# Kernel optimization log

Hardware: AMD Instinct MI355X
Metric: run time of the kernel (lower is better)

## Reference

```python
import jax, jax.numpy as jnp
import numpy as np

N, P, CF, K = 64, 1024, 16, 16  # batch, points, feature channels (after stripping 2 coord dims), knn K
BN_EPS = 1e-5


def _bn(x, g, b, m, v):
    # channel-last batchnorm in eval mode
    return (x - m) / jnp.sqrt(v + BN_EPS) * g + b


def _knn(pts, k):
    # pts: (N,P,2) -> indices of k nearest neighbors excluding self: (N,P,k)
    r = jnp.sum(pts * pts, axis=-1)                      # (N,P)
    d = r[:, :, None] - 2.0 * jnp.einsum('npc,nqc->npq', pts, pts) + r[:, None, :]
    _, idx = jax.lax.top_k(-d, k + 1)                    # (N,P,k+1)
    return idx[:, :, 1:]


def setup_inputs() -> dict:
    key = jax.random.key(0)
    ks = jax.random.split(key, 8)
    inp = {
        'features': jax.random.normal(ks[0], (N, P, 2 + CF), dtype=jnp.float32),
        'mask': jnp.zeros((N, P), dtype=bool),
        # edge conv stack: Conv2d(32->64), Conv2d(64->64), Conv2d(64->64), all 1x1
        'W0': jax.random.normal(ks[1], (64, 2 * CF), dtype=jnp.float32) / np.sqrt(2 * CF),
        'W1': jax.random.normal(ks[2], (64, 64), dtype=jnp.float32) / 8.0,
        'W2': jax.random.normal(ks[3], (64, 64), dtype=jnp.float32) / 8.0,
        # shortcut Conv1d(16->64)
        'Ws': jax.random.normal(ks[4], (64, CF), dtype=jnp.float32) / np.sqrt(CF),
    }
    for i, kk in zip(['0', '1', '2', 's'], jax.random.split(ks[5], 4)):
        k1, k2 = jax.random.split(kk)
        inp['g' + i] = jnp.ones((64,), jnp.float32)
        inp['b' + i] = jnp.zeros((64,), jnp.float32)
        inp['m' + i] = 0.1 * jax.random.normal(k1, (64,), jnp.float32)
        inp['v' + i] = jnp.ones((64,), jnp.float32) + 0.1 * jax.random.uniform(k2, (64,))
    return inp


def reference(features, mask, W0, W1, W2, Ws,
              g0, b0, m0, v0, g1, b1, m1, v1, g2, b2, m2, v2, gs, bs, ms, vs):
    pts = features[..., :2]          # (N,P,2)
    X = features[..., 2:]            # (N,P,CF)
    X_shortcut = X

    idx = _knn(pts, K)               # (N,P,K)
    f = jax.vmap(lambda x, i: x[i])(X, idx)              # gather neighbors: (N,P,K,CF)
    fc = jnp.broadcast_to(X[:, :, None, :], f.shape)     # center tiled
    h = jnp.concatenate([fc, fc - f], axis=-1)           # (N,P,K,2*CF)

    valid = mask.shape[1] - jnp.sum(mask, axis=1)        # (N,) number of valid points
    mask_K = idx >= valid[:, None, None]                 # (N,P,K) neighbor is padding

    for W, g, b, m, v in ((W0, g0, b0, m0, v0), (W1, g1, b1, m1, v1), (W2, g2, b2, m2, v2)):
        h = jax.nn.relu(_bn(jnp.einsum('npkc,oc->npko', h, W), g, b, m, v))

    h = jnp.where(mask_K[..., None], 0.0, h)             # (N,P,K,64)
    denom = jnp.maximum((K - jnp.sum(mask_K, axis=2)).astype(h.dtype), 1e-8)[..., None]
    agg = jnp.sum(h, axis=2) / denom                     # masked mean over K: (N,P,64)

    sc = _bn(jnp.einsum('npc,oc->npo', X_shortcut, Ws), gs, bs, ms, vs)
    sc = jnp.where(mask[..., None], 0.0, sc)

    out = jax.nn.relu(agg + sc)                          # (N,P,64)
    return jnp.transpose(out, (0, 2, 1))                 # (N,64,P) to match torch layout
```

## Files before the change

kernel.cpp:

```cpp
#include <hip/hip_runtime.h>

#define N_P 1024
#define N_K 16
#define C_IN 18

typedef _Float16 f16;
typedef f16 f16x8 __attribute__((ext_vector_type(8)));
typedef f16 f16x4 __attribute__((ext_vector_type(4)));
typedef float f32x4 __attribute__((ext_vector_type(4)));
typedef unsigned long long u64;

__global__ __launch_bounds__(256, 3) void fused_kernel(
    const float* __restrict__ feat, const unsigned char* __restrict__ mask,
    const float* __restrict__ W0, const float* __restrict__ W1,
    const float* __restrict__ W2, const float* __restrict__ Ws,
    const float* __restrict__ g0, const float* __restrict__ b0,
    const float* __restrict__ m0, const float* __restrict__ v0,
    const float* __restrict__ g1, const float* __restrict__ b1,
    const float* __restrict__ m1, const float* __restrict__ v1,
    const float* __restrict__ g2, const float* __restrict__ b2,
    const float* __restrict__ m2, const float* __restrict__ v2,
    const float* __restrict__ gs, const float* __restrict__ bs,
    const float* __restrict__ ms, const float* __restrict__ vs,
    float* __restrict__ out) {

    __shared__ __align__(16) char sbytes[16640 + 34816 + 16];
    float4* spts = (float4*)sbytes;
    float (*fbuf)[65] = (float(*)[65])sbytes;
    double* part = (double*)(sbytes + 16640);
    f16 (*hb)[16][72] = (f16(*)[16][72])(sbytes + 16640);
    int (*idx_lds)[16] = (int(*)[16])(sbytes + 16640 + 9216);
    int* msum = (int*)(sbytes + 16640 + 34816);

    const int tid = threadIdx.x;
    const int lane = tid & 63;
    const int w = tid >> 6;
    const int g = lane >> 4;
    const int c15 = lane & 15;
    const int n = blockIdx.x >> 4;
    const int P0 = (blockIdx.x & 15) << 6;
    const int PB = P0 + (w << 4);

    const float* fB = feat + (size_t)n * N_P * C_IN;

    if (tid == 0) *msum = 0;
    __syncthreads();
    for (int i = tid; i < N_P; i += 256) {
        float x = fB[i * C_IN + 0];
        float y = fB[i * C_IN + 1];
        float r = __fadd_rn(__fmul_rn(x, x), __fmul_rn(y, y));
        spts[i] = make_float4(x, y, r, 0.f);
    }
    {
        unsigned int m4 = *(const unsigned int*)(mask + (size_t)n * N_P + tid * 4);
        int part_c = (int)(((m4 & 0xFFu) != 0) + (((m4 >> 8) & 0xFFu) != 0) +
                           (((m4 >> 16) & 0xFFu) != 0) + (((m4 >> 24) & 0xFFu) != 0));
        atomicAdd(msum, part_c);
    }
    __syncthreads();
    const int valid = N_P - *msum;

    {
        const int q = lane;
        const int base = w << 8;
        const float4 me = spts[P0 + q];
        const float px = me.x, py = me.y, rp = me.z;

        double kk[17];
#pragma unroll
        for (int j = 0; j < 17; ++j) kk[j] = 0x1.0p60;

        double idx_d = (double)base;
        float4 nq = spts[base];
        for (int i = 0; i < 256; ++i) {
            const float4 qc = nq;
            nq = spts[base + ((i + 1) & 255)];
            float dot = __fadd_rn(__fmul_rn(px, qc.x), __fmul_rn(py, qc.y));
            float d   = __fadd_rn(__fsub_rn(rp, __fmul_rn(2.f, dot)), qc.z);
            unsigned int ud = __float_as_uint(d);
            ud ^= (unsigned int)((int)ud >> 31) | 0x80000000u;
            double x = fma((double)ud, 1024.0, idx_d);
            idx_d += 1.0;
#pragma unroll
            for (int j = 0; j < 17; ++j) {
                double lo = fmin(kk[j], x);
                x = fmax(kk[j], x);
                kk[j] = lo;
            }
        }
        double* pp = part + ((w << 6) + q) * 17;
#pragma unroll
        for (int j = 0; j < 17; ++j) pp[j] = kk[j];
    }
    __syncthreads();

    double fk[17];
    const bool owner = (lane < 16);
    {
#pragma unroll
        for (int j = 0; j < 17; ++j) fk[j] = 0x1.0p60;
        if (owner) {
            const int q = (w << 4) + lane;
            for (int s = 0; s < 4; ++s) {
                const double* pp = part + ((s << 6) + q) * 17;
#pragma unroll
                for (int j = 0; j < 17; ++j) {
                    double x = pp[j];
#pragma unroll
                    for (int jj = 0; jj < 17; ++jj) {
                        double lo = fmin(fk[jj], x);
                        x = fmax(fk[jj], x);
                        fk[jj] = lo;
                    }
                }
            }
        }
    }
    __syncthreads();
    if (owner) {
        const int q = (w << 4) + lane;
#pragma unroll
        for (int j = 1; j < 17; ++j) {
            double hi = trunc(fk[j] * 0x1.0p-10);
            idx_lds[q][j - 1] = (int)(fk[j] - hi * 1024.0);
        }
    }

    float tb0[4], tb1[4], tb2[4], tbs[4];
    f16x8 w0f[4], w1f[4][2], w2f[4][2];
    f16x4 wsf[4];
#pragma unroll
    for (int t = 0; t < 4; ++t) {
        const int o = t * 16 + c15;
        float s0 = g0[o] / sqrtf(v0[o] + 1e-5f);  tb0[t] = b0[o] - m0[o] * s0;
        float s1 = g1[o] / sqrtf(v1[o] + 1e-5f);  tb1[t] = b1[o] - m1[o] * s1;
        float s2 = g2[o] / sqrtf(v2[o] + 1e-5f);  tb2[t] = b2[o] - m2[o] * s2;
        float ss = gs[o] / sqrtf(vs[o] + 1e-5f);  tbs[t] = bs[o] - ms[o] * ss;
        const float* w0r = W0 + o * 32 + g * 8;
#pragma unroll
        for (int e = 0; e < 8; ++e) w0f[t][e] = (f16)(w0r[e] * s0);
        const float* w1r = W1 + o * 64 + g * 8;
        const float* w2r = W2 + o * 64 + g * 8;
#pragma unroll
        for (int ch = 0; ch < 2; ++ch)
#pragma unroll
            for (int e = 0; e < 8; ++e) {
                w1f[t][ch][e] = (f16)(w1r[ch * 32 + e] * s1);
                w2f[t][ch][e] = (f16)(w2r[ch * 32 + e] * s2);
            }
        const float* wsr = Ws + o * 16 + g * 4;
#pragma unroll
        for (int e = 0; e < 4; ++e) wsf[t][e] = (f16)(wsr[e] * ss);
    }

    for (int pp = 0; pp < 16; ++pp) {
        const int p = PB + pp;
        const int* ip = idx_lds[(w << 4) + pp];

        const int q = ip[c15];
        const int half = g & 1;
        const float* fcp = fB + p * C_IN + 2 + half * 8;
        float e0[8];
#pragma unroll
        for (int j = 0; j < 4; ++j) {
            float2 v = *(const float2*)(fcp + 2 * j);
            e0[2 * j] = v.x; e0[2 * j + 1] = v.y;
        }
        if (g >= 2) {
            const float* fqp = fB + q * C_IN + 2 + half * 8;
#pragma unroll
            for (int j = 0; j < 4; ++j) {
                float2 v = *(const float2*)(fqp + 2 * j);
                e0[2 * j] -= v.x; e0[2 * j + 1] -= v.y;
            }
        }
        f16x8 a0;
#pragma unroll
        for (int j = 0; j < 8; ++j) a0[j] = (f16)e0[j];

        f32x4 acc[4];
#pragma unroll
        for (int t = 0; t < 4; ++t) {
            acc[t] = (f32x4){tb0[t], tb0[t], tb0[t], tb0[t]};
            acc[t] = __builtin_amdgcn_mfma_f32_16x16x32_f16(a0, w0f[t], acc[t], 0, 0, 0);
        }
#pragma unroll
        for (int t = 0; t < 4; ++t)
#pragma unroll
            for (int r = 0; r < 4; ++r)
                hb[w][4 * g + r][t * 16 + c15] = (f16)fmaxf(acc[t][r], 0.f);

        f16x8 a1a = *(const f16x8*)&hb[w][c15][g * 8];
        f16x8 a1b = *(const f16x8*)&hb[w][c15][32 + g * 8];
        f32x4 acc1[4];
#pragma unroll
        for (int t = 0; t < 4; ++t) {
            acc1[t] = (f32x4){tb1[t], tb1[t], tb1[t], tb1[t]};
            acc1[t] = __builtin_amdgcn_mfma_f32_16x16x32_f16(a1a, w1f[t][0], acc1[t], 0, 0, 0);
            acc1[t] = __builtin_amdgcn_mfma_f32_16x16x32_f16(a1b, w1f[t][1], acc1[t], 0, 0, 0);
        }
#pragma unroll
        for (int t = 0; t < 4; ++t)
#pragma unroll
            for (int r = 0; r < 4; ++r)
                hb[w][4 * g + r][t * 16 + c15] = (f16)fmaxf(acc1[t][r], 0.f);

        f16x8 a2a = *(const f16x8*)&hb[w][c15][g * 8];
        f16x8 a2b = *(const f16x8*)&hb[w][c15][32 + g * 8];
        f32x4 acc2[4];
#pragma unroll
        for (int t = 0; t < 4; ++t) {
            acc2[t] = (f32x4){tb2[t], tb2[t], tb2[t], tb2[t]};
            acc2[t] = __builtin_amdgcn_mfma_f32_16x16x32_f16(a2a, w2f[t][0], acc2[t], 0, 0, 0);
            acc2[t] = __builtin_amdgcn_mfma_f32_16x16x32_f16(a2b, w2f[t][1], acc2[t], 0, 0, 0);
        }
        float ssum[4] = {0.f, 0.f, 0.f, 0.f};
        int cnt = 0;
#pragma unroll
        for (int r = 0; r < 4; ++r) {
            int qq = ip[4 * g + r];
            bool fl = (qq >= valid);
            cnt += fl ? 1 : 0;
#pragma unroll
            for (int t = 0; t < 4; ++t) {
                float v = fmaxf(acc2[t][r], 0.f);
                ssum[t] += fl ? 0.f : v;
            }
        }
#pragma unroll
        for (int t = 0; t < 4; ++t) {
            ssum[t] += __shfl_xor(ssum[t], 16);
            ssum[t] += __shfl_xor(ssum[t], 32);
        }
        cnt += __shfl_xor(cnt, 16);
        cnt += __shfl_xor(cnt, 32);
        float dn = fmaxf((float)(N_K - cnt), 1e-8f);
        if (g == 0) {
            int prow = (w << 4) + pp;
#pragma unroll
            for (int t = 0; t < 4; ++t)
                fbuf[prow][t * 16 + c15] = ssum[t] / dn;
        }
    }

    {
        const float* xr = fB + (size_t)(PB + c15) * C_IN + 2 + g * 4;
        float2 xa = *(const float2*)(xr);
        float2 xb = *(const float2*)(xr + 2);
        f16x4 as;
        as[0] = (f16)xa.x; as[1] = (f16)xa.y; as[2] = (f16)xb.x; as[3] = (f16)xb.y;
        f32x4 sacc[4];
#pragma unroll
        for (int t = 0; t < 4; ++t) {
            sacc[t] = (f32x4){tbs[t], tbs[t], tbs[t], tbs[t]};
            sacc[t] = __builtin_amdgcn_mfma_f32_16x16x16f16(as, wsf[t], sacc[t], 0, 0, 0);
        }
        const unsigned char* mrow = mask + (size_t)n * N_P + P0;
#pragma unroll
        for (int r = 0; r < 4; ++r) {
            int pl = (w << 4) + 4 * g + r;
            bool mk = (mrow[pl] != 0);
#pragma unroll
            for (int t = 0; t < 4; ++t) {
                float a = fbuf[pl][t * 16 + c15];
                float sv = mk ? 0.f : sacc[t][r];
                fbuf[pl][t * 16 + c15] = fmaxf(a + sv, 0.f);
            }
        }
    }
    __syncthreads();

    float* ob = out + (size_t)n * 64 * N_P + P0;
#pragma unroll
    for (int oo = 0; oo < 16; ++oo) {
        int o = (w << 4) + oo;
        ob[(size_t)o * N_P + lane] = fbuf[lane][o];
    }
}

extern "C" void kernel_launch(void* const* d_in, const int* in_sizes, int n_in,
                              void* d_out, int out_size, void* d_ws, size_t ws_size,
                              hipStream_t stream) {
    (void)in_sizes; (void)n_in; (void)out_size; (void)d_ws; (void)ws_size;
    const float* feat = (const float*)d_in[0];
    const unsigned char* mask = (const unsigned char*)d_in[1];
    const float* W0 = (const float*)d_in[2];
    const float* W1 = (const float*)d_in[3];
    const float* W2 = (const float*)d_in[4];
    const float* Ws = (const float*)d_in[5];
    const float* g0 = (const float*)d_in[6];
    const float* b0 = (const float*)d_in[7];
    const float* m0 = (const float*)d_in[8];
    const float* v0 = (const float*)d_in[9];
    const float* g1 = (const float*)d_in[10];
    const float* b1 = (const float*)d_in[11];
    const float* m1 = (const float*)d_in[12];
    const float* v1 = (const float*)d_in[13];
    const float* g2 = (const float*)d_in[14];
    const float* b2 = (const float*)d_in[15];
    const float* m2 = (const float*)d_in[16];
    const float* v2 = (const float*)d_in[17];
    const float* gs = (const float*)d_in[18];
    const float* bs = (const float*)d_in[19];
    const float* ms = (const float*)d_in[20];
    const float* vs = (const float*)d_in[21];
    float* out = (float*)d_out;

    fused_kernel<<<1024, 256, 0, stream>>>(feat, mask, W0, W1, W2, Ws,
                                           g0, b0, m0, v0, g1, b1, m1, v1,
                                           g2, b2, m2, v2, gs, bs, ms, vs,
                                           out);
}
```

Baseline: 297.8 us.

## Merge per-wave KNN partial lists with wave shuffles instead of shared memory

The KNN scan is remapped so each wave owns its 16 query points and its four lane-groups each scan a quarter of the candidates, with staggered start offsets to avoid LDS bank conflicts. The partial top-17 lists are merged with two xor-shuffle rounds in registers instead of being written to shared memory and merged serially by 16 owner lanes. This removes the 34 KB partial buffer and a barrier, so LDS use drops enough to raise launch bounds to 4 blocks per CU. The cost is that every lane now does the shuffle merges (more ALU work spread across all lanes), and register pressure may grow under the higher occupancy target.

Result: slower. 307.9 us (+3.4%).

```diff
diff --git a/kernel.cpp b/kernel.cpp
--- a/kernel.cpp
+++ b/kernel.cpp
@@ -8,9 +8,8 @@
 typedef f16 f16x8 __attribute__((ext_vector_type(8)));
 typedef f16 f16x4 __attribute__((ext_vector_type(4)));
 typedef float f32x4 __attribute__((ext_vector_type(4)));
-typedef unsigned long long u64;
-
-__global__ __launch_bounds__(256, 3) void fused_kernel(
+
+__global__ __launch_bounds__(256, 4) void fused_kernel(
     const float* __restrict__ feat, const unsigned char* __restrict__ mask,
     const float* __restrict__ W0, const float* __restrict__ W1,
     const float* __restrict__ W2, const float* __restrict__ Ws,
@@ -24,13 +23,12 @@
     const float* __restrict__ ms, const float* __restrict__ vs,
     float* __restrict__ out) {
 
-    __shared__ __align__(16) char sbytes[16640 + 34816 + 16];
+    __shared__ __align__(16) char sbytes[16640 + 9216 + 4096 + 16];
     float4* spts = (float4*)sbytes;
     float (*fbuf)[65] = (float(*)[65])sbytes;
-    double* part = (double*)(sbytes + 16640);
     f16 (*hb)[16][72] = (f16(*)[16][72])(sbytes + 16640);
     int (*idx_lds)[16] = (int(*)[16])(sbytes + 16640 + 9216);
-    int* msum = (int*)(sbytes + 16640 + 34816);
+    int* msum = (int*)(sbytes + 16640 + 9216 + 4096);
 
     const int tid = threadIdx.x;
     const int lane = tid & 63;
@@ -53,34 +51,36 @@
     }
     {
         unsigned int m4 = *(const unsigned int*)(mask + (size_t)n * N_P + tid * 4);
-        int part_c = (int)(((m4 & 0xFFu) != 0) + (((m4 >> 8) & 0xFFu) != 0) +
-                           (((m4 >> 16) & 0xFFu) != 0) + (((m4 >> 24) & 0xFFu) != 0));
-        atomicAdd(msum, part_c);
+        int mc = (int)(((m4 & 0xFFu) != 0) + (((m4 >> 8) & 0xFFu) != 0) +
+                       (((m4 >> 16) & 0xFFu) != 0) + (((m4 >> 24) & 0xFFu) != 0));
+        atomicAdd(msum, mc);
     }
     __syncthreads();
     const int valid = N_P - *msum;
 
+    double kk[17];
     {
-        const int q = lane;
-        const int base = w << 8;
-        const float4 me = spts[P0 + q];
+        const int qid = c15;
+        const int s = g;
+        const int base = s << 8;
+        const float4 me = spts[P0 + (w << 4) + qid];
         const float px = me.x, py = me.y, rp = me.z;
 
-        double kk[17];
 #pragma unroll
         for (int j = 0; j < 17; ++j) kk[j] = 0x1.0p60;
 
-        double idx_d = (double)base;
-        float4 nq = spts[base];
+        int off = (2 * s) & 255;
+        float4 nq = spts[base + off];
         for (int i = 0; i < 256; ++i) {
             const float4 qc = nq;
-            nq = spts[base + ((i + 1) & 255)];
+            const int cur = base + off;
+            off = (off + 1) & 255;
+            nq = spts[base + off];
             float dot = __fadd_rn(__fmul_rn(px, qc.x), __fmul_rn(py, qc.y));
-            float d   = __fadd_rn(__fsub_rn(rp, __fmul_rn(2.f, dot)), qc.z);
+            float d   = __fadd_rn(__builtin_fmaf(-2.f, dot, rp), qc.z);
             unsigned int ud = __float_as_uint(d);
             ud ^= (unsigned int)((int)ud >> 31) | 0x80000000u;
-            double x = fma((double)ud, 1024.0, idx_d);
-            idx_d += 1.0;
+            double x = __builtin_fma((double)ud, 1024.0, (double)cur);
 #pragma unroll
             for (int j = 0; j < 17; ++j) {
                 double lo = fmin(kk[j], x);
@@ -88,43 +88,33 @@
                 kk[j] = lo;
             }
         }
-        double* pp = part + ((w << 6) + q) * 17;
-#pragma unroll
-        for (int j = 0; j < 17; ++j) pp[j] = kk[j];
+#pragma unroll
+        for (int r = 0; r < 2; ++r) {
+            const int m = r == 0 ? 32 : 16;
+            double tmp[17];
+#pragma unroll
+            for (int j = 0; j < 17; ++j) tmp[j] = __shfl_xor(kk[j], m, 64);
+#pragma unroll
+            for (int j = 0; j < 17; ++j) {
+                double x = tmp[j];
+#pragma unroll
+                for (int jj = 0; jj < 17; ++jj) {
+                    double lo = fmin(kk[jj], x);
+                    x = fmax(kk[jj], x);
+                    kk[jj] = lo;
+                }
+            }
+        }
+        if (lane < 16) {
+            const int row = (w << 4) + qid;
+#pragma unroll
+            for (int j = 1; j < 17; ++j) {
+                double hi = __builtin_trunc(kk[j] * 0x1.0p-10);
+                idx_lds[row][j - 1] = (int)(kk[j] - hi * 1024.0);
+            }
+        }
     }
     __syncthreads();
-
-    double fk[17];
-    const bool owner = (lane < 16);
-    {
-#pragma unroll
-        for (int j = 0; j < 17; ++j) fk[j] = 0x1.0p60;
-        if (owner) {
-            const int q = (w << 4) + lane;
-            for (int s = 0; s < 4; ++s) {
-                const double* pp = part + ((s << 6) + q) * 17;
-#pragma unroll
-                for (int j = 0; j < 17; ++j) {
-                    double x = pp[j];
-#pragma unroll
-                    for (int jj = 0; jj < 17; ++jj) {
-                        double lo = fmin(fk[jj], x);
-                        x = fmax(fk[jj], x);
-                        fk[jj] = lo;
-                    }
-                }
-            }
-        }
-    }
-    __syncthreads();
-    if (owner) {
-        const int q = (w << 4) + lane;
-#pragma unroll
-        for (int j = 1; j < 17; ++j) {
-            double hi = trunc(fk[j] * 0x1.0p-10);
-            idx_lds[q][j - 1] = (int)(fk[j] - hi * 1024.0);
-        }
-    }
 
     float tb0[4], tb1[4], tb2[4], tbs[4];
     f16x8 w0f[4], w1f[4][2], w2f[4][2];
```
